# Kernel optimization log

Hardware: AMD Instinct MI355X
Metric: run time of the kernel (lower is better)

The kernel has to match this reference:

```python
import jax, jax.numpy as jnp
import numpy as np

NEIGHBOR_NUM = 50
SUPPORT = 1  # support_num

def _normalize(x, axis):
    n = jnp.linalg.norm(x, axis=axis, keepdims=True)
    return x / jnp.maximum(n, 1e-12)

def get_neighbor_index(v, k):
    # v: (b, n, 3) -> kNN indices (b, n, k), excluding self (smallest distance)
    inner = jnp.einsum('bvd,bwd->bvw', v, v)
    q = jnp.sum(v * v, axis=-1)
    dist = -2.0 * inner + q[:, None, :] + q[:, :, None]  # (b, n, n)
    _, idx = jax.lax.top_k(-dist, k + 1)                 # smallest k+1
    return idx[:, :, 1:]

def indexing_neighbor(t, idx):
    # t: (b, n, c), idx: (b, n, k) -> (b, n, k, c)
    return jax.vmap(lambda tb, ib: tb[ib])(t, idx)

def neighbor_direction_norm(v, idx):
    nbr = indexing_neighbor(v, idx)                      # (b, n, k, 3)
    return _normalize(nbr - v[:, :, None, :], -1)

def conv_surface(idx, v, directions, kernel_num):
    b, vn, nn_ = idx.shape
    dnorm = neighbor_direction_norm(v, idx)              # (b, n, k, 3)
    sdir = _normalize(directions, 0)                     # (3, s*kern)
    theta = jax.nn.relu(jnp.einsum('bvnd,dk->bvnk', dnorm, sdir))
    theta = theta.reshape(b, vn, nn_, SUPPORT, kernel_num)
    return jnp.sum(jnp.max(theta, axis=2), axis=2)       # (b, n, kern)

def conv_layer(idx, v, fmap, weights, bias, directions, out_c):
    b, vn, nn_ = idx.shape
    dnorm = neighbor_direction_norm(v, idx)
    sdir = _normalize(directions, 0)                     # (3, s*out)
    theta = jax.nn.relu(jnp.einsum('bvnd,dk->bvnk', dnorm, sdir))  # (b,n,k,s*out)
    fout = fmap @ weights + bias                         # (b, n, (s+1)*out)
    f_center = fout[:, :, :out_c]
    f_support = indexing_neighbor(fout[:, :, out_c:], idx)         # (b,n,k,s*out)
    act = (theta * f_support).reshape(b, vn, nn_, SUPPORT, out_c)
    return f_center + jnp.sum(jnp.max(act, axis=2), axis=2)

def pool(v, fmap, rate=4, nnum=4):
    idx = get_neighbor_index(v, nnum)
    pooled = jnp.max(indexing_neighbor(fmap, idx), axis=2)
    pn = v.shape[1] // rate
    sel = jnp.arange(pn)  # deterministic subsample (original: randperm)
    return v[:, sel, :], pooled[:, sel, :]

def _uniform(key, shape, stdv):
    return jax.random.uniform(key, shape, jnp.float32, -stdv, stdv)

def setup_inputs() -> dict:
    key = jax.random.key(0)
    ks = jax.random.split(key, 20)
    import math
    d = {'vertices': jax.random.normal(ks[0], (2, 8192, 3), jnp.float32)}
    # Conv_surface(kernel_num=32)
    d['dir0'] = _uniform(ks[1], (3, SUPPORT * 32), 1.0 / math.sqrt(SUPPORT * 32))
    def mk(kw, kb, kd, in_c, out_c):
        s = 1.0 / math.sqrt(out_c * (SUPPORT + 1))
        return (_uniform(kw, (in_c, (SUPPORT + 1) * out_c), s),
                _uniform(kb, ((SUPPORT + 1) * out_c,), s),
                _uniform(kd, (3, SUPPORT * out_c), s))
    d['w1'], d['b1'], d['d1'] = mk(ks[2], ks[3], ks[4], 32, 64)
    d['w2'], d['b2'], d['d2'] = mk(ks[5], ks[6], ks[7], 64, 128)
    d['w3'], d['b3'], d['d3'] = mk(ks[8], ks[9], ks[10], 128, 256)
    d['w4'], d['b4'], d['d4'] = mk(ks[11], ks[12], ks[13], 256, 1024)
    fstd = 1.0 / math.sqrt(1024)
    d['fc_w'] = _uniform(ks[14], (1024, 256), fstd)
    d['fc_b'] = _uniform(ks[15], (256,), fstd)
    return d

def reference(vertices, dir0, w1, b1, d1, w2, b2, d2, w3, b3, d3, w4, b4, d4, fc_w, fc_b):
    v = vertices
    idx = get_neighbor_index(v, NEIGHBOR_NUM)
    fm0 = jax.nn.relu(conv_surface(idx, v, dir0, 32))
    fm1 = jax.nn.relu(conv_layer(idx, v, fm0, w1, b1, d1, 64))
    v, fm1 = pool(v, fm1)
    idx = get_neighbor_index(v, NEIGHBOR_NUM)
    fm2 = jax.nn.relu(conv_layer(idx, v, fm1, w2, b2, d2, 128))
    fm3 = jax.nn.relu(conv_layer(idx, v, fm2, w3, b3, d3, 256))
    v, fm3 = pool(v, fm3)
    idx = get_neighbor_index(v, NEIGHBOR_NUM)
    fm4 = conv_layer(idx, v, fm3, w4, b4, d4, 1024)
    feat = jnp.max(fm4, axis=1)                          # (b, 1024)
    return feat @ fc_w + fc_b                            # (b, 256)
```

## Files before the change

kernel.cpp:

```cpp
#include <hip/hip_runtime.h>
#include <cmath>


__device__ __forceinline__ unsigned flipf(float f) {
    unsigned u = __float_as_uint(f);
    return (u & 0x80000000u) ? ~u : (u | 0x80000000u);
}
__device__ __forceinline__ float unflip(unsigned u) {
    unsigned r = (u & 0x80000000u) ? (u & 0x7fffffffu) : ~u;
    return __uint_as_float(r);
}
__device__ __forceinline__ unsigned umin2(unsigned a, unsigned b) {
    return a < b ? a : b;
}

template <int VC>
__device__ __forceinline__ void load_vec(float* d, const float* p) {
    if constexpr (VC == 1) { d[0] = p[0]; }
    else if constexpr (VC == 2) { const float2 t = *(const float2*)p; d[0] = t.x; d[1] = t.y; }
    else { const float4 t = *(const float4*)p; d[0] = t.x; d[1] = t.y; d[2] = t.z; d[3] = t.w; }
}
template <int VC>
__device__ __forceinline__ void store_vec(float* p, const float* d) {
    if constexpr (VC == 1) { p[0] = d[0]; }
    else if constexpr (VC == 2) { float2 t; t.x = d[0]; t.y = d[1]; *(float2*)p = t; }
    else { float4 t; t.x = d[0]; t.y = d[1]; t.z = d[2]; t.w = d[3]; *(float4*)p = t; }
}

__global__ __launch_bounds__(256) void precompute_vq(
    const float* __restrict__ v, float4* __restrict__ vq, int n)
{
#pragma clang fp contract(off)
    const int i = blockIdx.x * 256 + threadIdx.x;
    if (i < n) {
        const float x = v[i * 3 + 0];
        const float y = v[i * 3 + 1];
        const float z = v[i * 3 + 2];
        float4 o; o.x = x; o.y = y; o.z = z; o.w = (x * x + y * y) + z * z;
        vq[i] = o;
    }
}

template <int CPT, int SMP, int SEL, int EST, int QPB = 8, int CAPQ = 160>
__global__ __launch_bounds__(256, 4) void knn_select(
    const float4* __restrict__ vq, int vStride, int nRows,
    int* __restrict__ outIdx)
{
#pragma clang fp contract(off)
    const int tid  = threadIdx.x;
    const int bpb  = nRows / QPB;
    const int b    = blockIdx.x / bpb;
    const int row0 = (blockIdx.x % bpb) * QPB;
    const float4* vb = vq + (size_t)b * vStride;

    float nx[QPB], ny[QPB], nz[QPB], qw[QPB];
#pragma unroll
    for (int qq = 0; qq < QPB; ++qq) {
        const float4 p = vb[row0 + qq];
        nx[qq] = p.x * -2.0f; ny[qq] = p.y * -2.0f; nz[qq] = p.z * -2.0f;
        qw[qq] = p.w;
    }

    float mn[QPB];
#pragma unroll
    for (int qq = 0; qq < QPB; ++qq) mn[qq] = INFINITY;
#pragma unroll
    for (int s = 0; s < SMP; ++s) {
        const float4 c = vb[tid + (s << 8)];
#pragma unroll
        for (int qq = 0; qq < QPB; ++qq) {
            const float t0 = (nx[qq] * c.x + ny[qq] * c.y) + nz[qq] * c.z;
            const float dist = (t0 + c.w) + qw[qq];
            mn[qq] = fminf(mn[qq], dist);
        }
    }

    constexpr int POOLB = (QPB * CAPQ * 8 > CPT * SEL * 6) ? QPB * CAPQ * 8
                                                           : CPT * SEL * 6;
    __shared__ unsigned hmin[QPB][256];
    __shared__ __align__(16) char poolmem[POOLB];
    __shared__ unsigned Ts[QPB];
    __shared__ int cnt[QPB];
    __shared__ unsigned T2_s;
    __shared__ int fcnt;
    typedef unsigned long long u64row[CAPQ];
    u64row* bufq = (u64row*)poolmem;

#pragma unroll
    for (int qq = 0; qq < QPB; ++qq) hmin[qq][tid] = flipf(mn[qq]);
    if (tid < QPB) { Ts[tid] = 0u; cnt[tid] = 0; }
    __syncthreads();

    {
        const int g = tid >> 5, l = tid & 31;
#pragma unroll
        for (int hh = 0; hh < 2; ++hh) {
            const int i = l + hh * 32;
            unsigned cm = hmin[g][i];
            cm = umin2(cm, hmin[g][i + 64]);
            cm = umin2(cm, hmin[g][i + 128]);
            cm = umin2(cm, hmin[g][i + 192]);
            hmin[g][i] = cm;
        }
#pragma unroll
        for (int hh = 0; hh < 2; ++hh) {
            const unsigned vv = hmin[g][l + hh * 32];
            int r = 0;
#pragma unroll 8
            for (int k = 0; k < 64; ++k) r += (hmin[g][k] < vv) ? 1 : 0;
            if (r < EST) atomicMax(&Ts[g], vv);
        }
    }
    __syncthreads();

    float Tf[QPB];
#pragma unroll
    for (int qq = 0; qq < QPB; ++qq) Tf[qq] = unflip(Ts[qq]);

    {
        constexpr int PF = (CPT < 4) ? CPT : 4;
        float4 cbuf[PF];
#pragma unroll
        for (int p = 0; p < PF; ++p) cbuf[p] = vb[tid + (p << 8)];
        for (int s0 = 0; s0 < CPT; s0 += PF) {
            float4 cur[PF];
#pragma unroll
            for (int p = 0; p < PF; ++p) cur[p] = cbuf[p];
            if (s0 + PF < CPT) {
#pragma unroll
                for (int p = 0; p < PF; ++p)
                    cbuf[p] = vb[tid + ((s0 + PF + p) << 8)];
            }
#pragma unroll
            for (int p = 0; p < PF; ++p) {
                const int j = tid + ((s0 + p) << 8);
                const float4 c = cur[p];
#pragma unroll
                for (int qq = 0; qq < QPB; ++qq) {
                    const float t0 = (nx[qq] * c.x + ny[qq] * c.y) + nz[qq] * c.z;
                    const float dist = (t0 + c.w) + qw[qq];
                    if (dist <= Tf[qq]) {
                        const int p2 = atomicAdd(&cnt[qq], 1);
                        if (p2 < CAPQ)
                            bufq[qq][p2] =
                                (((unsigned long long)flipf(dist)) << 32)
                                | (unsigned)j;
                    }
                }
            }
        }
    }
    __syncthreads();

    {
        const int g = tid >> 5, i = tid & 31;
        const int M = cnt[g];
        if (M >= SEL && M <= CAPQ) {
            for (int s2 = i; s2 < M; s2 += 32) {
                const unsigned long long k = bufq[g][s2];
                int rr = 0;
                for (int i2 = 0; i2 < M; ++i2) rr += (bufq[g][i2] < k) ? 1 : 0;
                if (rr >= 1 && rr < SEL)
                    outIdx[(size_t)(b * nRows + row0 + g) * (SEL - 1) + (rr - 1)]
                        = (int)(k & 0xffffffffu);
            }
        }
    }
    __syncthreads();

    for (int qq = 0; qq < QPB; ++qq) {
        const int M = cnt[qq];
        if (M >= SEL && M <= CAPQ) continue;
        unsigned* fD = (unsigned*)poolmem;
        unsigned short* fJ = (unsigned short*)(poolmem + CPT * SEL * 4);
        {
            float fm = INFINITY;
#pragma unroll 2
            for (int s = 0; s < CPT; ++s) {
                const float4 c = vb[tid + (s << 8)];
                const float t0 = (nx[qq] * c.x + ny[qq] * c.y) + nz[qq] * c.z;
                const float dist = (t0 + c.w) + qw[qq];
                fm = fminf(fm, dist);
            }
            hmin[qq][tid] = flipf(fm);
        }
        if (tid == 0) { T2_s = 0u; fcnt = 0; }
        __syncthreads();
        {
            const unsigned vv = hmin[qq][tid];
            int r = 0;
            for (int k = 0; k < 256; ++k) r += (hmin[qq][k] < vv) ? 1 : 0;
            if (r < SEL) atomicMax(&T2_s, vv);
        }
        __syncthreads();
        const float T2f = unflip(T2_s);
#pragma unroll 2
        for (int s = 0; s < CPT; ++s) {
            const int j = tid + (s << 8);
            const float4 c = vb[j];
            const float t0 = (nx[qq] * c.x + ny[qq] * c.y) + nz[qq] * c.z;
            const float dist = (t0 + c.w) + qw[qq];
            if (dist <= T2f) {
                const int p = atomicAdd(&fcnt, 1);
                fD[p] = flipf(dist);
                fJ[p] = (unsigned short)j;
            }
        }
        __syncthreads();
        const int M2 = fcnt;
        for (int s2 = tid; s2 < M2; s2 += 256) {
            const unsigned dk = fD[s2];
            const unsigned short jk = fJ[s2];
            int rr = 0;
            for (int i2 = 0; i2 < M2; ++i2) {
                const unsigned di = fD[i2];
                rr += (di < dk || (di == dk && fJ[i2] < jk)) ? 1 : 0;
            }
            if (rr >= 1 && rr < SEL)
                outIdx[(size_t)(b * nRows + row0 + qq) * (SEL - 1) + (rr - 1)]
                    = (int)jk;
        }
        __syncthreads();
    }
}

template <int NT, int VC>
__global__ __launch_bounds__(NT) void conv_kernel(
    const int*    __restrict__ idx,
    const float4* __restrict__ vq,
    int vStride, int V, int NN,
    const float* __restrict__ fout,
    int oc,
    const float* __restrict__ dirs,
    float* __restrict__ out,
    int do_relu)
{
    constexpr int G = NT / 64;
    __shared__ float dnx[G][64], dny[G][64], dnz[G][64];
    __shared__ int   nb[G][64];
    const int w    = threadIdx.x >> 6;
    const int lane = threadIdx.x & 63;
    const int vi   = blockIdx.x * G + w;
    const int b    = vi / V;
    const int i    = vi % V;

    if (lane < NN) {
        const int j = idx[(size_t)vi * NN + lane];
        nb[w][lane] = j;
        const float4 ci = vq[(size_t)b * vStride + i];
        const float4 cj = vq[(size_t)b * vStride + j];
        const float dx = cj.x - ci.x;
        const float dy = cj.y - ci.y;
        const float dz = cj.z - ci.z;
        const float n  = sqrtf((dx * dx + dy * dy) + dz * dz);
        const float dnv = fmaxf(n, 1e-12f);
        dnx[w][lane] = dx / dnv;
        dny[w][lane] = dy / dnv;
        dnz[w][lane] = dz / dnv;
    }
    __syncthreads();

    const int c0 = blockIdx.y * (64 * VC) + lane * VC;
    if (c0 >= oc) return;

    float d0[VC], d1[VC], d2[VC], fcen[VC], m[VC];
#pragma unroll
    for (int k = 0; k < VC; ++k) {
        const float a  = dirs[c0 + k];
        const float bb = dirs[oc + c0 + k];
        const float cc = dirs[2 * oc + c0 + k];
        const float nd = sqrtf((a * a + bb * bb) + cc * cc);
        const float dc = fmaxf(nd, 1e-12f);
        d0[k] = a / dc; d1[k] = bb / dc; d2[k] = cc / dc;
        fcen[k] = 0.f;
        m[k] = -INFINITY;
    }
    const float* fsup = nullptr;
    if (fout) {
        fsup = fout + (size_t)b * V * (2 * oc) + oc;
        load_vec<VC>(fcen, &fout[(size_t)vi * (2 * oc) + c0]);
    }

    constexpr int BN = (VC >= 4) ? 5 : 10;
    for (int n0 = 0; n0 < 50; n0 += BN) {
        float fs[BN][VC];
        if (fsup) {
#pragma unroll
            for (int u = 0; u < BN; ++u)
                load_vec<VC>(fs[u], &fsup[(size_t)nb[w][n0 + u] * (2 * oc) + c0]);
        } else {
#pragma unroll
            for (int u = 0; u < BN; ++u)
#pragma unroll
                for (int k = 0; k < VC; ++k) fs[u][k] = 1.f;
        }
#pragma unroll
        for (int u = 0; u < BN; ++u) {
            const int n = n0 + u;
            const float ax = dnx[w][n], ay = dny[w][n], az = dnz[w][n];
#pragma unroll
            for (int k = 0; k < VC; ++k) {
                float th = (ax * d0[k] + ay * d1[k]) + az * d2[k];
                th = fmaxf(th, 0.f);
                m[k] = fmaxf(m[k], th * fs[u][k]);
            }
        }
    }
    float r[VC];
#pragma unroll
    for (int k = 0; k < VC; ++k) {
        r[k] = fcen[k] + m[k];
        if (do_relu) r[k] = fmaxf(r[k], 0.f);
    }
    store_vec<VC>(&out[(size_t)vi * oc + c0], r);
}

__global__ __launch_bounds__(256) void gemm_tiled(
    const float* __restrict__ A, const float* __restrict__ W,
    const float* __restrict__ bias, float* __restrict__ out,
    int M, int K, int N)
{
    __shared__ float As[32][68];
    __shared__ float Bs[32][64];
    const int tid = threadIdx.x;
    const int tx = tid & 15, ty = tid >> 4;
    const int r0 = blockIdx.x * 64;
    const int c0 = blockIdx.y * 64;

    const float4 bv = *(const float4*)&bias[c0 + tx * 4];
    float acc[4][4];
#pragma unroll
    for (int i = 0; i < 4; ++i) {
        acc[i][0] = bv.x; acc[i][1] = bv.y; acc[i][2] = bv.z; acc[i][3] = bv.w;
    }

    const int rowA = tid >> 2;
    const int ca4  = tid & 3;
    const int rowB = tid >> 4;
    const int cb4  = tid & 15;

    for (int k0 = 0; k0 < K; k0 += 32) {
        const float4 a0 = *(const float4*)&A[(size_t)(r0 + rowA) * K + k0 + ca4 * 4];
        const float4 a1 = *(const float4*)&A[(size_t)(r0 + rowA) * K + k0 + (ca4 + 4) * 4];
        const float4 b0 = *(const float4*)&W[(size_t)(k0 + rowB) * N + c0 + cb4 * 4];
        const float4 b1 = *(const float4*)&W[(size_t)(k0 + rowB + 16) * N + c0 + cb4 * 4];
        __syncthreads();
        As[ca4 * 4 + 0][rowA] = a0.x;
        As[ca4 * 4 + 1][rowA] = a0.y;
        As[ca4 * 4 + 2][rowA] = a0.z;
        As[ca4 * 4 + 3][rowA] = a0.w;
        As[ca4 * 4 + 16][rowA] = a1.x;
        As[ca4 * 4 + 17][rowA] = a1.y;
        As[ca4 * 4 + 18][rowA] = a1.z;
        As[ca4 * 4 + 19][rowA] = a1.w;
        *(float4*)&Bs[rowB][cb4 * 4]      = b0;
        *(float4*)&Bs[rowB + 16][cb4 * 4] = b1;
        __syncthreads();
#pragma unroll
        for (int kk = 0; kk < 32; ++kk) {
            const float4 av = *(const float4*)&As[kk][ty * 4];
            const float4 wv = *(const float4*)&Bs[kk][tx * 4];
            acc[0][0] += av.x * wv.x; acc[0][1] += av.x * wv.y;
            acc[0][2] += av.x * wv.z; acc[0][3] += av.x * wv.w;
            acc[1][0] += av.y * wv.x; acc[1][1] += av.y * wv.y;
            acc[1][2] += av.y * wv.z; acc[1][3] += av.y * wv.w;
            acc[2][0] += av.z * wv.x; acc[2][1] += av.z * wv.y;
            acc[2][2] += av.z * wv.z; acc[2][3] += av.z * wv.w;
            acc[3][0] += av.w * wv.x; acc[3][1] += av.w * wv.y;
            acc[3][2] += av.w * wv.z; acc[3][3] += av.w * wv.w;
        }
    }
#pragma unroll
    for (int i = 0; i < 4; ++i) {
        float4 o;
        o.x = acc[i][0]; o.y = acc[i][1]; o.z = acc[i][2]; o.w = acc[i][3];
        *(float4*)&out[(size_t)(r0 + ty * 4 + i) * N + c0 + tx * 4] = o;
    }
}

__global__ __launch_bounds__(256) void pool_max(
    const int* __restrict__ idxNN, int nnStride, const float* __restrict__ fm,
    int Vin, int pn, int C, float* __restrict__ out)
{
    const int t  = blockIdx.x * 256 + threadIdx.x;
    const int c  = t % C;
    const int bi = t / C;
    const int b  = bi / pn;
    const int i  = bi % pn;
    const int* r = idxNN + (size_t)(b * Vin + i) * nnStride;
    const int j0 = r[0], j1 = r[1], j2 = r[2], j3 = r[3];
    float m = fm[((size_t)b * Vin + j0) * C + c];
    m = fmaxf(m, fm[((size_t)b * Vin + j1) * C + c]);
    m = fmaxf(m, fm[((size_t)b * Vin + j2) * C + c]);
    m = fmaxf(m, fm[((size_t)b * Vin + j3) * C + c]);
    out[(size_t)bi * C + c] = m;
}

__global__ __launch_bounds__(256) void colmax_part(
    const float* __restrict__ fm, int V, int C, int rowsPerChunk,
    float* __restrict__ part)
{
    const int b = blockIdx.y, chunk = blockIdx.z;
    const int nChunk = gridDim.z;
    const int c = blockIdx.x * 256 + threadIdx.x;
    const int i0 = chunk * rowsPerChunk;
    float m = -INFINITY;
    for (int i = i0; i < i0 + rowsPerChunk; ++i)
        m = fmaxf(m, fm[((size_t)b * V + i) * C + c]);
    part[((size_t)b * nChunk + chunk) * C + c] = m;
}

__global__ __launch_bounds__(256) void fc_kernel(
    const float* __restrict__ part, const float* __restrict__ W,
    const float* __restrict__ bias, float* __restrict__ out, int nChunk)
{
    __shared__ float f[1024];
    const int b = blockIdx.x, tid = threadIdx.x;
    for (int k = tid; k < 1024; k += 256) {
        float m = part[((size_t)b * nChunk) * 1024 + k];
        for (int ch = 1; ch < nChunk; ++ch)
            m = fmaxf(m, part[((size_t)b * nChunk + ch) * 1024 + k]);
        f[k] = m;
    }
    __syncthreads();
    float acc = bias[tid];
    for (int k = 0; k < 1024; ++k) acc += f[k] * W[(size_t)k * 256 + tid];
    out[(size_t)b * 256 + tid] = acc;
}

extern "C" void kernel_launch(void* const* d_in, const int* in_sizes, int n_in,
                              void* d_out, int out_size, void* d_ws, size_t ws_size,
                              hipStream_t stream) {
    const float* verts = (const float*)d_in[0];
    const float* dir0  = (const float*)d_in[1];
    const float* w1 = (const float*)d_in[2];
    const float* b1 = (const float*)d_in[3];
    const float* d1 = (const float*)d_in[4];
    const float* w2 = (const float*)d_in[5];
    const float* b2 = (const float*)d_in[6];
    const float* d2 = (const float*)d_in[7];
    const float* w3 = (const float*)d_in[8];
    const float* b3 = (const float*)d_in[9];
    const float* d3 = (const float*)d_in[10];
    const float* w4 = (const float*)d_in[11];
    const float* b4 = (const float*)d_in[12];
    const float* d4 = (const float*)d_in[13];
    const float* fcw = (const float*)d_in[14];
    const float* fcb = (const float*)d_in[15];

    const int B = 2, V1 = 8192, V2 = 2048, V3 = 512, NN = 50;

    char* ws = (char*)d_ws;
    float*  arena1 = (float*)(ws + 0);
    float*  arena2 = (float*)(ws + 8388608);
    float*  arena3 = (float*)(ws + 12582912);
    int*    arena4 = (int*)  (ws + 16777216);
    float*  arena5 = (float*)(ws + 20054016);
    float*  arena6 = (float*)(ws + 22151168);
    float*  part   = (float*)(ws + 23265280);
    float4* vq     = (float4*)(ws + 23330816);

    precompute_vq<<<(B * V1 + 255) / 256, 256, 0, stream>>>(verts, vq, B * V1);

    int* idxA = arena4;
    knn_select<32, 8, 51, 20><<<B * V1 / 8, 256, 0, stream>>>(vq, V1, V1, idxA);

    float* fm0 = arena5;
    conv_kernel<256, 1><<<dim3(B * V1 / 4, 1), 256, 0, stream>>>(
        idxA, vq, V1, V1, NN, nullptr, 32, dir0, fm0, 1);
    float* fout1 = arena1;
    gemm_tiled<<<dim3(B * V1 / 64, 128 / 64), 256, 0, stream>>>(
        fm0, w1, b1, fout1, B * V1, 32, 128);
    float* fm1 = arena2;
    conv_kernel<256, 1><<<dim3(B * V1 / 4, 1), 256, 0, stream>>>(
        idxA, vq, V1, V1, NN, fout1, 64, d1, fm1, 1);
    float* fm1p = arena6;
    pool_max<<<B * V2 * 64 / 256, 256, 0, stream>>>(idxA, NN, fm1, V1, V2, 64, fm1p);

    int* idxB = arena4;
    knn_select<8, 2, 51, 20><<<B * V2 / 8, 256, 0, stream>>>(vq, V1, V2, idxB);
    float* fout2 = arena3;
    gemm_tiled<<<dim3(B * V2 / 64, 256 / 64), 256, 0, stream>>>(
        fm1p, w2, b2, fout2, B * V2, 64, 256);
    float* fm2 = arena5;
    conv_kernel<256, 2><<<dim3(B * V2 / 4, 1), 256, 0, stream>>>(
        idxB, vq, V1, V2, NN, fout2, 128, d2, fm2, 1);
    float* fout3 = arena1;
    gemm_tiled<<<dim3(B * V2 / 64, 512 / 64), 256, 0, stream>>>(
        fm2, w3, b3, fout3, B * V2, 128, 512);
    float* fm3 = arena2;
    conv_kernel<256, 4><<<dim3(B * V2 / 4, 1), 256, 0, stream>>>(
        idxB, vq, V1, V2, NN, fout3, 256, d3, fm3, 1);
    float* fm3p = arena6;
    pool_max<<<B * V3 * 256 / 256, 256, 0, stream>>>(idxB, NN, fm3, V2, V3, 256, fm3p);

    int* idxC = arena4;
    knn_select<2, 2, 51, 48><<<B * V3 / 8, 256, 0, stream>>>(vq, V1, V3, idxC);
    float* fout4 = arena1;
    gemm_tiled<<<dim3(B * V3 / 64, 2048 / 64), 256, 0, stream>>>(
        fm3p, w4, b4, fout4, B * V3, 256, 2048);
    float* fm4 = arena2;
    conv_kernel<256, 4><<<dim3(B * V3 / 4, 4), 256, 0, stream>>>(
        idxC, vq, V1, V3, NN, fout4, 1024, d4, fm4, 0);
    colmax_part<<<dim3(1024 / 256, B, 8), 256, 0, stream>>>(fm4, V3, 1024, V3 / 8, part);
    fc_kernel<<<B, 256, 0, stream>>>(part, fcw, fcb, (float*)d_out, 8);
}
```

Before: 347.2 us.

## Register-block kNN rank counts and pack two vertices per wave in surface conv

The kNN threshold estimation now counts ranks for both candidate values in one pass over shared memory. The exact top-k ranking keeps each thread's keys in registers and sweeps the buffer once instead of once per key. The surface conv (oc=32) previously left half of each 64-lane wave idle; it now maps two vertices per wave with 32 lanes each and launches half as many blocks. Costs are extra registers for the unrolled key arrays and a more complex neighbor-setup loop.

```diff
diff --git a/kernel.cpp b/kernel.cpp
--- a/kernel.cpp
+++ b/kernel.cpp
@@ -102,14 +102,17 @@
             cm = umin2(cm, hmin[g][i + 192]);
             hmin[g][i] = cm;
         }
-#pragma unroll
-        for (int hh = 0; hh < 2; ++hh) {
-            const unsigned vv = hmin[g][l + hh * 32];
-            int r = 0;
+        const unsigned vv0 = hmin[g][l];
+        const unsigned vv1 = hmin[g][l + 32];
+        int r0 = 0, r1 = 0;
 #pragma unroll 8
-            for (int k = 0; k < 64; ++k) r += (hmin[g][k] < vv) ? 1 : 0;
-            if (r < EST) atomicMax(&Ts[g], vv);
-        }
+        for (int k = 0; k < 64; ++k) {
+            const unsigned h = hmin[g][k];
+            r0 += (h < vv0) ? 1 : 0;
+            r1 += (h < vv1) ? 1 : 0;
+        }
+        if (r0 < EST) atomicMax(&Ts[g], vv0);
+        if (r1 < EST) atomicMax(&Ts[g], vv1);
     }
     __syncthreads();
 
@@ -156,13 +159,25 @@
         const int g = tid >> 5, i = tid & 31;
         const int M = cnt[g];
         if (M >= SEL && M <= CAPQ) {
-            for (int s2 = i; s2 < M; s2 += 32) {
-                const unsigned long long k = bufq[g][s2];
-                int rr = 0;
-                for (int i2 = 0; i2 < M; ++i2) rr += (bufq[g][i2] < k) ? 1 : 0;
-                if (rr >= 1 && rr < SEL)
-                    outIdx[(size_t)(b * nRows + row0 + g) * (SEL - 1) + (rr - 1)]
-                        = (int)(k & 0xffffffffu);
+            constexpr int KMAX = (CAPQ + 31) / 32;
+            unsigned long long myk[KMAX];
+            int rr[KMAX];
+#pragma unroll
+            for (int t = 0; t < KMAX; ++t) {
+                const int s2 = i + t * 32;
+                myk[t] = (s2 < M) ? bufq[g][s2] : ~0ull;
+                rr[t] = 0;
+            }
+            for (int i2 = 0; i2 < M; ++i2) {
+                const unsigned long long k2 = bufq[g][i2];
+#pragma unroll
+                for (int t = 0; t < KMAX; ++t) rr[t] += (k2 < myk[t]) ? 1 : 0;
+            }
+#pragma unroll
+            for (int t = 0; t < KMAX; ++t) {
+                if (rr[t] >= 1 && rr[t] < SEL)
+                    outIdx[(size_t)(b * nRows + row0 + g) * (SEL - 1) + (rr[t] - 1)]
+                        = (int)(myk[t] & 0xffffffffu);
             }
         }
     }
@@ -224,7 +239,7 @@
     }
 }
 
-template <int NT, int VC>
+template <int NT, int VC, int VPW = 1>
 __global__ __launch_bounds__(NT) void conv_kernel(
     const int*    __restrict__ idx,
     const float4* __restrict__ vq,
@@ -235,32 +250,42 @@
     float* __restrict__ out,
     int do_relu)
 {
-    constexpr int G = NT / 64;
-    __shared__ float dnx[G][64], dny[G][64], dnz[G][64];
-    __shared__ int   nb[G][64];
-    const int w    = threadIdx.x >> 6;
-    const int lane = threadIdx.x & 63;
-    const int vi   = blockIdx.x * G + w;
-    const int b    = vi / V;
-    const int i    = vi % V;
-
-    if (lane < NN) {
-        const int j = idx[(size_t)vi * NN + lane];
-        nb[w][lane] = j;
-        const float4 ci = vq[(size_t)b * vStride + i];
-        const float4 cj = vq[(size_t)b * vStride + j];
-        const float dx = cj.x - ci.x;
-        const float dy = cj.y - ci.y;
-        const float dz = cj.z - ci.z;
-        const float n  = sqrtf((dx * dx + dy * dy) + dz * dz);
-        const float dnv = fmaxf(n, 1e-12f);
-        dnx[w][lane] = dx / dnv;
-        dny[w][lane] = dy / dnv;
-        dnz[w][lane] = dz / dnv;
+    constexpr int NWAVE = NT / 64;
+    constexpr int NV    = NWAVE * VPW;
+    __shared__ float dnx[NV][64], dny[NV][64], dnz[NV][64];
+    __shared__ int   nb[NV][64];
+
+    for (int t = threadIdx.x; t < NV * 64; t += NT) {
+        const int vloc = t >> 6, lane2 = t & 63;
+        if (lane2 < NN) {
+            const int vi = blockIdx.x * NV + vloc;
+            const int b  = vi / V;
+            const int i  = vi % V;
+            const int j  = idx[(size_t)vi * NN + lane2];
+            nb[vloc][lane2] = j;
+            const float4 ci = vq[(size_t)b * vStride + i];
+            const float4 cj = vq[(size_t)b * vStride + j];
+            const float dx = cj.x - ci.x;
+            const float dy = cj.y - ci.y;
+            const float dz = cj.z - ci.z;
+            const float n  = sqrtf((dx * dx + dy * dy) + dz * dz);
+            const float dnv = fmaxf(n, 1e-12f);
+            dnx[vloc][lane2] = dx / dnv;
+            dny[vloc][lane2] = dy / dnv;
+            dnz[vloc][lane2] = dz / dnv;
+        }
     }
     __syncthreads();
 
-    const int c0 = blockIdx.y * (64 * VC) + lane * VC;
+    const int w     = threadIdx.x >> 6;
+    const int lane  = threadIdx.x & 63;
+    const int sub   = (VPW == 1) ? 0 : (lane >> 5);
+    const int laneC = (VPW == 1) ? lane : (lane & 31);
+    const int vloc  = w * VPW + sub;
+    const int vi    = blockIdx.x * NV + vloc;
+    const int b     = vi / V;
+
+    const int c0 = blockIdx.y * ((64 / VPW) * VC) + laneC * VC;
     if (c0 >= oc) return;
 
     float d0[VC], d1[VC], d2[VC], fcen[VC], m[VC];
@@ -287,7 +312,7 @@
         if (fsup) {
 #pragma unroll
             for (int u = 0; u < BN; ++u)
-                load_vec<VC>(fs[u], &fsup[(size_t)nb[w][n0 + u] * (2 * oc) + c0]);
+                load_vec<VC>(fs[u], &fsup[(size_t)nb[vloc][n0 + u] * (2 * oc) + c0]);
         } else {
 #pragma unroll
             for (int u = 0; u < BN; ++u)
@@ -297,7 +322,7 @@
 #pragma unroll
         for (int u = 0; u < BN; ++u) {
             const int n = n0 + u;
-            const float ax = dnx[w][n], ay = dny[w][n], az = dnz[w][n];
+            const float ax = dnx[vloc][n], ay = dny[vloc][n], az = dnz[vloc][n];
 #pragma unroll
             for (int k = 0; k < VC; ++k) {
                 float th = (ax * d0[k] + ay * d1[k]) + az * d2[k];
@@ -466,7 +491,7 @@
     knn_select<32, 8, 51, 20><<<B * V1 / 8, 256, 0, stream>>>(vq, V1, V1, idxA);
 
     float* fm0 = arena5;
-    conv_kernel<256, 1><<<dim3(B * V1 / 4, 1), 256, 0, stream>>>(
+    conv_kernel<256, 1, 2><<<dim3(B * V1 / 8, 1), 256, 0, stream>>>(
         idxA, vq, V1, V1, NN, nullptr, 32, dir0, fm0, 1);
     float* fout1 = arena1;
     gemm_tiled<<<dim3(B * V1 / 64, 128 / 64), 256, 0, stream>>>(
```

After: 334.0 us. 3.8% less time.
